# Optimization experiments

Hardware: AMD Instinct MI355X
Metric: run time of the kernel (lower is better)

The kernel has to match this reference:

```python
import jax, jax.numpy as jnp
import numpy as np

B = 131072   # batch
D = 64       # latent_dim
P = 32       # n_pairs
H = 64       # hidden_dim
EMA = 1.0    # ema buffer initial value (detached in original, so a constant)


def setup_inputs() -> dict:
    key = jax.random.key(0)
    ks = jax.random.split(key, 4)
    z = jax.random.normal(ks[0], (B, D), dtype=jnp.float32)
    # tiny MLP params (2 -> H -> H -> 1), small init so exp(score) stays finite
    W1 = jax.random.normal(ks[1], (2, H), dtype=jnp.float32) * 0.05
    b1 = jnp.zeros((H,), jnp.float32)
    W2 = jax.random.normal(ks[2], (H, H), dtype=jnp.float32) * 0.05
    b2 = jnp.zeros((H,), jnp.float32)
    W3 = jax.random.normal(ks[3], (H, 1), dtype=jnp.float32) * 0.05
    b3 = jnp.zeros((1,), jnp.float32)
    # sampled dimension pairs: randperm(D)[:2] sorted, per pair
    rng = np.random.default_rng(0)
    idx = np.argsort(rng.random((P, D)), axis=1)[:, :2]
    pairs = jnp.asarray(np.sort(idx, axis=1).astype(np.int32))
    # per-pair batch permutations (randperm(B))
    perms = jnp.asarray(np.argsort(rng.random((P, B)), axis=1).astype(np.int32))
    return {"z": z, "W1": W1, "b1": b1, "W2": W2, "b2": b2,
            "W3": W3, "b3": b3, "pairs": pairs, "perms": perms}


def _mlp(x, W1, b1, W2, b2, W3, b3):
    # x: [P, B, 2] -> scores [P, B]
    h = jax.nn.elu(x @ W1 + b1)
    h = jax.nn.elu(h @ W2 + b2)
    return (h @ W3 + b3)[..., 0]


def reference(z, W1, b1, W2, b2, W3, b3, pairs, perms):
    # gather latent dims for all pairs at once: [P, B]
    z_i = z[:, pairs[:, 0]].T
    z_j = z[:, pairs[:, 1]].T
    z_i_sh = jnp.take_along_axis(z_i, perms, axis=1)  # shuffled marginals
    joint_in = jnp.stack([z_i, z_j], axis=-1)      # [P, B, 2]
    marg_in = jnp.stack([z_i_sh, z_j], axis=-1)    # [P, B, 2]
    joint = _mlp(joint_in, W1, b1, W2, b2, W3, b3)  # [P, B]
    marg = _mlp(marg_in, W1, b1, W2, b2, W3, b3)    # [P, B]
    et = jnp.mean(jnp.exp(marg), axis=1)            # [P]
    mi = jnp.mean(joint, axis=1) - jnp.log(et / EMA)
    return jnp.mean(mi)
```

## Files before the change

kernel.cpp:

```cpp
#include <hip/hip_runtime.h>
#include <hip/hip_bf16.h>
#include <math.h>

#define B_N   131072
#define D_DIM 64
#define P_N   32
#define H_DIM 64
#define TPB   256
#define GRIDX 64
#define SPB   (B_N / GRIDX)
#define SPI   128
#define ITERS (SPB / SPI)

#define K_L2E 1.44269504088896340736f
#define LN2F  0.693147180559945309f

typedef __attribute__((ext_vector_type(8))) short bf16x8;
typedef __attribute__((ext_vector_type(4))) float f32x4;

static __device__ __forceinline__ unsigned short bfbits(float f) {
    __hip_bfloat16 b = __float2bfloat16(f);
    unsigned short u; __builtin_memcpy(&u, &b, 2); return u;
}
static __device__ __forceinline__ float bf2f(unsigned short u) {
    return __uint_as_float(((unsigned)u) << 16);
}

__global__ void transpose_z(const float* __restrict__ z, float* __restrict__ zT) {
    __shared__ float tile[64][65];
    const int s0 = blockIdx.x * 64;
    const int t  = threadIdx.x;
    #pragma unroll
    for (int it = 0; it < 4; ++it) {
        int r  = it * 16 + (t >> 4);
        int c4 = (t & 15) * 4;
        const float4 v = *(const float4*)&z[(long)(s0 + r) * 64 + c4];
        tile[r][c4 + 0] = v.x; tile[r][c4 + 1] = v.y;
        tile[r][c4 + 2] = v.z; tile[r][c4 + 3] = v.w;
    }
    __syncthreads();
    #pragma unroll
    for (int it = 0; it < 16; ++it) {
        int d = it * 4 + (t >> 6);
        int s = t & 63;
        zT[d * B_N + s0 + s] = tile[s][d];
    }
}

__global__ void prep_weights(const float* __restrict__ W2,
                             unsigned short* __restrict__ w2hi,
                             unsigned short* __restrict__ w2lo) {
    int t = blockIdx.x * blockDim.x + threadIdx.x;
    int m = t & 7, l = (t >> 3) & 63, n = (t >> 9) & 3, c = t >> 11;
    int k = c * 32 + (l >> 4) * 8 + m;
    int col = n * 16 + (l & 15);
    float v = W2[k * 64 + col];
    unsigned short hi = bfbits(v);
    unsigned short lo = bfbits(v - bf2f(hi));
    w2hi[t] = hi;
    w2lo[t] = lo;
}

static __device__ __forceinline__ float eluK(float xk) {
    float neg = fmaf(__builtin_amdgcn_exp2f(xk), K_L2E, -K_L2E);
    return __builtin_amdgcn_fmed3f(xk, neg, 0.0f);
}

union Frag { unsigned u[4]; bf16x8 v; };

template<int ET, int TR>
__global__ __launch_bounds__(TPB, 2)
void mine_mfma(const float* __restrict__ zp,
               const float* __restrict__ W1, const float* __restrict__ b1,
               const unsigned short* __restrict__ w2hi,
               const unsigned short* __restrict__ w2lo,
               const float* __restrict__ b2,
               const float* __restrict__ W3,
               const int* __restrict__ pairs, const int* __restrict__ perms,
               double* __restrict__ partials) {
    const int wg = blockIdx.x;
    const int lg = (wg & 7) * (P_N * GRIDX / 8) + (wg >> 3);
    const int p  = lg >> 6;
    const int bx = lg & (GRIDX - 1);

    const int i    = pairs[2 * p];
    const int j    = pairs[2 * p + 1];
    const int tid  = threadIdx.x;
    const int lane = tid & 63;
    const int wv   = tid >> 6;
    const int g    = lane >> 4;
    const int r16  = lane & 15;

    #define ZA(idx) (TR ? zp[(long)i * B_N + (idx)] : zp[(long)(idx) * 64 + i])
    #define ZB(idx) (TR ? zp[(long)j * B_N + (idx)] : zp[(long)(idx) * 64 + j])

    float w1a[2][8], w1b[2][8], b1v[2][8];
    #pragma unroll
    for (int c = 0; c < 2; ++c)
        #pragma unroll
        for (int m = 0; m < 8; ++m) {
            int d = c * 32 + g * 8 + m;
            w1a[c][m] = W1[d]      * K_L2E;
            w1b[c][m] = W1[64 + d] * K_L2E;
            b1v[c][m] = b1[d]      * K_L2E;
        }

    const bf16x8* fh = (const bf16x8*)w2hi;
    const bf16x8* fl = (const bf16x8*)w2lo;
    bf16x8 wh[2][4], wl[2][4];
    #pragma unroll
    for (int c = 0; c < 2; ++c)
        #pragma unroll
        for (int n = 0; n < 4; ++n) {
            wh[c][n] = fh[(c * 4 + n) * 64 + lane];
            wl[c][n] = fl[(c * 4 + n) * 64 + lane];
        }

    float b2v[4], w3v[4];
    #pragma unroll
    for (int n = 0; n < 4; ++n) {
        b2v[n] = b2[n * 16 + r16] * K_L2E;
        w3v[n] = ET ? W3[n * 16 + r16]
                    : W3[n * 16 + r16] * LN2F;
    }

    const int  sbase = bx * SPB + wv * 16 + r16;
    const int* pperm = perms + (long)p * B_N;
    #define SIDX(t, u) (sbase + (t) * SPI + (u) * 64)

    float aC[2], bC[2], aN[2], bN[2];
    int   pmN2[2];
    #pragma unroll
    for (int u = 0; u < 2; ++u) {
        const int s0 = SIDX(0, u);
        const int s1 = SIDX(1, u);
        int pm0 = ET ? pperm[s0] : s0;
        int pm1 = ET ? pperm[s1] : s1;
        bC[u] = ZB(s0);  aC[u] = ZA(pm0);
        bN[u] = ZB(s1);  aN[u] = ZA(pm1);
        pmN2[u] = ET ? pperm[SIDX(2, u)] : SIDX(2, u);
    }

    double acd0 = 0.0, acd1 = 0.0;

    for (int t = 0; t < ITERS; ++t) {
        const int t2 = (t + 2 < ITERS) ? t + 2 : ITERS - 1;
        const int t3 = (t + 3 < ITERS) ? t + 3 : ITERS - 1;
        int   pmN3[2];
        float bN2[2], aN2[2];
        #pragma unroll
        for (int u = 0; u < 2; ++u) {
            pmN3[u] = ET ? pperm[SIDX(t3, u)] : SIDX(t3, u);
            bN2[u]  = ZB(SIDX(t2, u));
            aN2[u]  = ZA(pmN2[u]);
        }

        Frag ah[2][2], al[2][2];
        #pragma unroll
        for (int u = 0; u < 2; ++u)
            #pragma unroll
            for (int c = 0; c < 2; ++c)
                #pragma unroll
                for (int w = 0; w < 4; ++w) {
                    float pe = fmaf(aC[u], w1a[c][2*w],   fmaf(bC[u], w1b[c][2*w],   b1v[c][2*w]));
                    float po = fmaf(aC[u], w1a[c][2*w+1], fmaf(bC[u], w1b[c][2*w+1], b1v[c][2*w+1]));
                    float he = eluK(pe);
                    float ho = eluK(po);
                    unsigned ue = __float_as_uint(he), uo = __float_as_uint(ho);
                    ah[u][c].u[w] = __builtin_amdgcn_perm(uo, ue, 0x07060302u);
                    float le = he - __uint_as_float(ue & 0xFFFF0000u);
                    float lf = ho - __uint_as_float(uo & 0xFFFF0000u);
                    al[u][c].u[w] = __builtin_amdgcn_perm(__float_as_uint(lf),
                                                          __float_as_uint(le), 0x07060302u);
                }

        f32x4 acc[2][4];
        #pragma unroll
        for (int u = 0; u < 2; ++u)
            #pragma unroll
            for (int n = 0; n < 4; ++n)
                acc[u][n] = (f32x4){b2v[n], b2v[n], b2v[n], b2v[n]};
        #pragma unroll
        for (int u = 0; u < 2; ++u)
            #pragma unroll
            for (int c = 0; c < 2; ++c) {
                #pragma unroll
                for (int n = 0; n < 4; ++n)
                    acc[u][n] = __builtin_amdgcn_mfma_f32_16x16x32_bf16(ah[u][c].v, wh[c][n], acc[u][n], 0, 0, 0);
                #pragma unroll
                for (int n = 0; n < 4; ++n)
                    acc[u][n] = __builtin_amdgcn_mfma_f32_16x16x32_bf16(ah[u][c].v, wl[c][n], acc[u][n], 0, 0, 0);
                #pragma unroll
                for (int n = 0; n < 4; ++n)
                    acc[u][n] = __builtin_amdgcn_mfma_f32_16x16x32_bf16(al[u][c].v, wh[c][n], acc[u][n], 0, 0, 0);
            }

        float sc[2][4];
        #pragma unroll
        for (int u = 0; u < 2; ++u) {
            sc[u][0] = sc[u][1] = sc[u][2] = sc[u][3] = 0.f;
            #pragma unroll
            for (int r = 0; r < 4; ++r)
                #pragma unroll
                for (int n = 0; n < 4; ++n)
                    sc[u][r] = fmaf(eluK(acc[u][n][r]), w3v[n], sc[u][r]);
        }

        if (ET == 0) {
            acd0 += (double)((sc[0][0] + sc[0][1]) + (sc[0][2] + sc[0][3]));
            acd1 += (double)((sc[1][0] + sc[1][1]) + (sc[1][2] + sc[1][3]));
        } else {
            #pragma unroll
            for (int u = 0; u < 2; ++u) {
                const bool o1 = lane & 1;
                float k01 = o1 ? sc[u][1] : sc[u][0];
                float s01 = o1 ? sc[u][0] : sc[u][1];
                float v01 = k01 + __shfl_xor(s01, 1, 64);
                float k23 = o1 ? sc[u][3] : sc[u][2];
                float s23 = o1 ? sc[u][2] : sc[u][3];
                float v23 = k23 + __shfl_xor(s23, 1, 64);
                const bool o2 = lane & 2;
                float kk = o2 ? v23 : v01;
                float ss = o2 ? v01 : v23;
                float v  = kk + __shfl_xor(ss, 2, 64);
                v += __shfl_xor(v, 4, 64);
                v += __shfl_xor(v, 8, 64);
                float ev = __builtin_amdgcn_exp2f(v);
                if (u == 0) acd0 += (double)ev;
                else        acd1 += (double)ev;
            }
        }

        #pragma unroll
        for (int u = 0; u < 2; ++u) {
            aC[u] = aN[u]; bC[u] = bN[u];
            aN[u] = aN2[u]; bN[u] = bN2[u];
            pmN2[u] = pmN3[u];
        }
    }

    double accd = acd0 + acd1;

    __shared__ double red[TPB];
    red[tid] = accd;
    __syncthreads();
    for (int s = TPB / 2; s > 0; s >>= 1) {
        if (tid < s) red[tid] += red[tid + s];
        __syncthreads();
    }
    if (tid == 0) {
        double v = (ET == 0) ? red[0] : red[0] * 0.25;
        partials[ET * (P_N * GRIDX) + p * GRIDX + bx] = v;
    }
    #undef ZA
    #undef ZB
    #undef SIDX
}

__global__ void mine_final(const double* __restrict__ partials, float* __restrict__ out) {
    int lane = threadIdx.x;
    double mi = 0.0;
    if (lane < P_N) {
        double sj = 0.0, sm = 0.0;
        for (int c = 0; c < GRIDX; ++c) {
            sj += partials[lane * GRIDX + c];
            sm += partials[P_N * GRIDX + lane * GRIDX + c];
        }
        mi = sj / (double)B_N - log(sm / (double)B_N);
    }
    #pragma unroll
    for (int off = 32; off > 0; off >>= 1) mi += __shfl_down(mi, off);
    if (lane == 0) out[0] = (float)(mi / (double)P_N);
}

extern "C" void kernel_launch(void* const* d_in, const int* in_sizes, int n_in,
                              void* d_out, int out_size, void* d_ws, size_t ws_size,
                              hipStream_t stream) {
    const float* z     = (const float*)d_in[0];
    const float* W1    = (const float*)d_in[1];
    const float* b1    = (const float*)d_in[2];
    const float* W2    = (const float*)d_in[3];
    const float* b2    = (const float*)d_in[4];
    const float* W3    = (const float*)d_in[5];
    const int*   pairs = (const int*)d_in[7];
    const int*   perms = (const int*)d_in[8];

    const size_t ZT_BYTES = (size_t)D_DIM * B_N * sizeof(float);
    const bool   tr = ws_size >= ZT_BYTES + 65536;

    float* zT   = (float*)d_ws;
    char*  wb   = (char*)d_ws + (tr ? ZT_BYTES : 0);
    unsigned short* w2hi = (unsigned short*)wb;
    unsigned short* w2lo = (unsigned short*)(wb + 8192);
    double* partials     = (double*)(wb + 16384);

    prep_weights<<<16, 256, 0, stream>>>(W2, w2hi, w2lo);

    dim3 grid(P_N * GRIDX, 1, 1);
    if (tr) {
        transpose_z<<<B_N / 64, 256, 0, stream>>>(z, zT);
        mine_mfma<0, 1><<<grid, TPB, 0, stream>>>(zT, W1, b1, w2hi, w2lo, b2, W3,
                                                  pairs, perms, partials);
        mine_mfma<1, 1><<<grid, TPB, 0, stream>>>(zT, W1, b1, w2hi, w2lo, b2, W3,
                                                  pairs, perms, partials);
    } else {
        mine_mfma<0, 0><<<grid, TPB, 0, stream>>>(z, W1, b1, w2hi, w2lo, b2, W3,
                                                  pairs, perms, partials);
        mine_mfma<1, 0><<<grid, TPB, 0, stream>>>(z, W1, b1, w2hi, w2lo, b2, W3,
                                                  pairs, perms, partials);
    }
    mine_final<<<1, 64, 0, stream>>>(partials, (float*)d_out);
}
```

Baseline: 289.5 us.

## Stage W2 fragments in LDS and raise occupancy to four blocks per SM

Moves the hi/lo bf16 W2 fragments out of per-thread registers into a shared LDS buffer loaded once per block, and reloads them from LDS inside the MFMA loop. The launch bound goes from 2 to 4 blocks so the freed registers allow more resident waves to hide latency. The MFMA loop is reordered by output column so each set of weight fragments is read once per n. The cost is extra LDS reads per iteration and a block barrier at startup, plus some risk of spills under the tighter register budget.

Measured after the change: 443.7 us. 1.53x slower.

```diff
diff --git a/kernel.cpp b/kernel.cpp
--- a/kernel.cpp
+++ b/kernel.cpp
@@ -69,7 +69,7 @@
 union Frag { unsigned u[4]; bf16x8 v; };
 
 template<int ET, int TR>
-__global__ __launch_bounds__(TPB, 2)
+__global__ __launch_bounds__(TPB, 4)
 void mine_mfma(const float* __restrict__ zp,
                const float* __restrict__ W1, const float* __restrict__ b1,
                const unsigned short* __restrict__ w2hi,
@@ -94,6 +94,17 @@
     #define ZA(idx) (TR ? zp[(long)i * B_N + (idx)] : zp[(long)(idx) * 64 + i])
     #define ZB(idx) (TR ? zp[(long)j * B_N + (idx)] : zp[(long)(idx) * 64 + j])
 
+    __shared__ bf16x8 w2s[1024];
+    {
+        const bf16x8* gh = (const bf16x8*)w2hi;
+        const bf16x8* gl = (const bf16x8*)w2lo;
+        #pragma unroll
+        for (int q = 0; q < 4; ++q) {
+            int idx = q * TPB + tid;
+            w2s[idx] = (idx < 512) ? gh[idx] : gl[idx - 512];
+        }
+    }
+
     float w1a[2][8], w1b[2][8], b1v[2][8];
     #pragma unroll
     for (int c = 0; c < 2; ++c)
@@ -105,17 +116,6 @@
             b1v[c][m] = b1[d]      * K_L2E;
         }
 
-    const bf16x8* fh = (const bf16x8*)w2hi;
-    const bf16x8* fl = (const bf16x8*)w2lo;
-    bf16x8 wh[2][4], wl[2][4];
-    #pragma unroll
-    for (int c = 0; c < 2; ++c)
-        #pragma unroll
-        for (int n = 0; n < 4; ++n) {
-            wh[c][n] = fh[(c * 4 + n) * 64 + lane];
-            wl[c][n] = fl[(c * 4 + n) * 64 + lane];
-        }
-
     float b2v[4], w3v[4];
     #pragma unroll
     for (int n = 0; n < 4; ++n) {
@@ -123,6 +123,8 @@
         w3v[n] = ET ? W3[n * 16 + r16]
                     : W3[n * 16 + r16] * LN2F;
     }
+
+    __syncthreads();
 
     const int  sbase = bx * SPB + wv * 16 + r16;
     const int* pperm = perms + (long)p * B_N;
@@ -174,6 +176,8 @@
                                                           __float_as_uint(le), 0x07060302u);
                 }
 
+        asm volatile("" ::: "memory");
+
         f32x4 acc[2][4];
         #pragma unroll
         for (int u = 0; u < 2; ++u)
@@ -181,19 +185,21 @@
             for (int n = 0; n < 4; ++n)
                 acc[u][n] = (f32x4){b2v[n], b2v[n], b2v[n], b2v[n]};
         #pragma unroll
-        for (int u = 0; u < 2; ++u)
-            #pragma unroll
-            for (int c = 0; c < 2; ++c) {
-                #pragma unroll
-                for (int n = 0; n < 4; ++n)
-                    acc[u][n] = __builtin_amdgcn_mfma_f32_16x16x32_bf16(ah[u][c].v, wh[c][n], acc[u][n], 0, 0, 0);
-                #pragma unroll
-                for (int n = 0; n < 4; ++n)
-                    acc[u][n] = __builtin_amdgcn_mfma_f32_16x16x32_bf16(ah[u][c].v, wl[c][n], acc[u][n], 0, 0, 0);
-                #pragma unroll
-                for (int n = 0; n < 4; ++n)
-                    acc[u][n] = __builtin_amdgcn_mfma_f32_16x16x32_bf16(al[u][c].v, wh[c][n], acc[u][n], 0, 0, 0);
+        for (int n = 0; n < 4; ++n) {
+            bf16x8 wh0 = w2s[      n * 64 + lane];
+            bf16x8 wl0 = w2s[512 + n * 64 + lane];
+            bf16x8 wh1 = w2s[      (4 + n) * 64 + lane];
+            bf16x8 wl1 = w2s[512 + (4 + n) * 64 + lane];
+            #pragma unroll
+            for (int u = 0; u < 2; ++u) {
+                acc[u][n] = __builtin_amdgcn_mfma_f32_16x16x32_bf16(ah[u][0].v, wh0, acc[u][n], 0, 0, 0);
+                acc[u][n] = __builtin_amdgcn_mfma_f32_16x16x32_bf16(ah[u][0].v, wl0, acc[u][n], 0, 0, 0);
+                acc[u][n] = __builtin_amdgcn_mfma_f32_16x16x32_bf16(al[u][0].v, wh0, acc[u][n], 0, 0, 0);
+                acc[u][n] = __builtin_amdgcn_mfma_f32_16x16x32_bf16(ah[u][1].v, wh1, acc[u][n], 0, 0, 0);
+                acc[u][n] = __builtin_amdgcn_mfma_f32_16x16x32_bf16(ah[u][1].v, wl1, acc[u][n], 0, 0, 0);
+                acc[u][n] = __builtin_amdgcn_mfma_f32_16x16x32_bf16(al[u][1].v, wh1, acc[u][n], 0, 0, 0);
             }
+        }
 
         float sc[2][4];
         #pragma unroll
```
